# Performance work log

Hardware: AMD Instinct MI355X
Metric: run time of the kernel (lower is better)

The kernel has to match this reference:

```python
import jax, jax.numpy as jnp
import numpy as np

B_SZ, L, D, N = 2, 2048, 1024, 16


def setup_inputs() -> dict:
    key = jax.random.key(0)
    ks = jax.random.split(key, 6)
    x = jax.random.normal(ks[0], (B_SZ, L, D), dtype=jnp.float32)
    W_b = jax.random.normal(ks[1], (N, D), dtype=jnp.float32) * (1.0 / np.sqrt(D))
    W_c = jax.random.normal(ks[2], (N, D), dtype=jnp.float32) * (1.0 / np.sqrt(D))
    # scaled so softplus(s_delta) stays in a sane range (avoids exp overflow)
    W_delta = jax.random.normal(ks[3], (1, D), dtype=jnp.float32) * 0.02
    # negative A (standard for stable SSMs) keeps exp(Delta*A) bounded
    A = -jnp.abs(jax.random.normal(ks[4], (D, N), dtype=jnp.float32))
    delta_param = jax.random.normal(ks[5], (D,), dtype=jnp.float32) * 0.1
    return {"x": x, "W_b": W_b, "W_c": W_c, "W_delta": W_delta, "A": A, "delta_param": delta_param}


def reference(x, W_b, W_c, W_delta, A, delta_param):
    # Input-dependent projections (torch Linear: x @ W.T)
    B = jnp.einsum("bld,nd->bln", x, W_b)                      # [b,l,n]
    C = jnp.einsum("bld,nd->bln", x, W_c)                      # [b,l,n]
    s_delta = jnp.einsum("bld,od->blo", x, W_delta)            # [b,l,1]
    # repeat_interleave(d) of a length-1 axis == broadcast over d
    Delta = jax.nn.softplus(s_delta + delta_param)             # [b,l,d]
    # ZOH discretization
    dA = Delta[..., None] * A                                  # [b,l,d,n]
    A_bar = jnp.exp(dA)                                        # [b,l,d,n]
    B_bar = (A_bar - 1.0) / dA * (Delta[..., None] * B[:, :, None, :])  # [b,l,d,n]
    deltaB_x = B_bar * x[..., None]                            # [b,l,d,n]
    # pack all computed quantities into one array: [b,l,2d+1,n]
    return jnp.concatenate([A_bar, deltaB_x, C[:, :, None, :]], axis=2)
```

## Files before the change

### kernel.cpp

```cpp
#include <hip/hip_runtime.h>
#include <cmath>

#define D_DIM 1024
#define N_DIM 16
#define KTOT  2049
#define WS_STRIDE 36

typedef float v4f __attribute__((ext_vector_type(4)));

__global__ __launch_bounds__(256) void proj_kernel(
    const float* __restrict__ x, const float* __restrict__ W_b,
    const float* __restrict__ W_c, const float* __restrict__ W_delta,
    float* __restrict__ ws, float* __restrict__ out)
{
    const int bl   = blockIdx.x;
    const int tid  = threadIdx.x;
    const int wave = tid >> 6;
    const int lane = tid & 63;

    const float* xrow  = x + (size_t)bl * D_DIM;
    const float* Wbase = (wave < 2) ? W_b : W_c;
    const int rowbase  = (wave & 1) * 8;

    float acc[8] = {0.f,0.f,0.f,0.f,0.f,0.f,0.f,0.f};
    float sd = 0.f;

    for (int i = 0; i < D_DIM / 64; ++i) {
        const int d = lane + (i << 6);
        const float xv = xrow[d];
        #pragma unroll
        for (int r = 0; r < 8; ++r)
            acc[r] = fmaf(xv, Wbase[(rowbase + r) * D_DIM + d], acc[r]);
        if (wave == 0) sd = fmaf(xv, W_delta[d], sd);
    }

    #pragma unroll
    for (int r = 0; r < 8; ++r) {
        #pragma unroll
        for (int m = 32; m >= 1; m >>= 1)
            acc[r] += __shfl_xor(acc[r], m, 64);
    }
    if (wave == 0) {
        #pragma unroll
        for (int m = 32; m >= 1; m >>= 1)
            sd += __shfl_xor(sd, m, 64);
    }

    if (lane == 0) {
        if (wave < 2) {
            float* dst = ws + (size_t)bl * WS_STRIDE + rowbase;
            #pragma unroll
            for (int r = 0; r < 8; ++r) dst[r] = acc[r];
            if (wave == 0) ws[(size_t)bl * WS_STRIDE + 32] = sd;
        } else {
            float* dst = out + ((size_t)bl * KTOT + 2 * D_DIM) * N_DIM + rowbase;
            #pragma unroll
            for (int r = 0; r < 8; ++r) dst[r] = acc[r];
        }
    }
}

__global__ __launch_bounds__(256) void ssm_kernel(
    const float* __restrict__ x, const float* __restrict__ A,
    const float* __restrict__ delta_param, const float* __restrict__ ws,
    float* __restrict__ out)
{
    const int blk   = blockIdx.x;
    const int bl    = blk >> 4;
    const int chunk = blk & 15;
    const int tid   = threadIdx.x;
    const int n4    = tid & 3;
    const int dloc  = tid >> 2;
    const int d     = (chunk << 6) + dloc;

    const float sd = ws[bl * WS_STRIDE + 32];
    const v4f   Bv = *(const v4f*)(ws + bl * WS_STRIDE + (n4 << 2));
    const float dp = delta_param[d];
    const v4f   Av = *(const v4f*)(A + (size_t)d * N_DIM + (n4 << 2));
    const float xv = x[(size_t)bl * D_DIM + d];

    const float z     = sd + dp;
    const float Delta = fmaxf(z, 0.0f) + log1pf(expf(-fabsf(z)));
    const float dx    = Delta * xv;

    v4f Abar, dbx;
    #pragma unroll
    for (int i = 0; i < 4; ++i) {
        const float dA = Delta * Av[i];
        const float em = expm1f(dA);
        Abar[i] = em + 1.0f;
        const float ratio = (dA != 0.0f) ? (em / dA) : 1.0f;
        dbx[i] = ratio * Bv[i] * dx;
    }

    const size_t base = ((size_t)bl * KTOT + d) * N_DIM + (n4 << 2);
    __builtin_nontemporal_store(Abar, (v4f*)(out + base));
    __builtin_nontemporal_store(dbx,  (v4f*)(out + base + (size_t)D_DIM * N_DIM));
}

extern "C" void kernel_launch(void* const* d_in, const int* in_sizes, int n_in,
                              void* d_out, int out_size, void* d_ws, size_t ws_size,
                              hipStream_t stream)
{
    const float* x           = (const float*)d_in[0];
    const float* W_b         = (const float*)d_in[1];
    const float* W_c         = (const float*)d_in[2];
    const float* W_delta     = (const float*)d_in[3];
    const float* A           = (const float*)d_in[4];
    const float* delta_param = (const float*)d_in[5];
    float* out = (float*)d_out;
    float* ws  = (float*)d_ws;

    const int BL = in_sizes[0] / D_DIM;

    proj_kernel<<<BL, 256, 0, stream>>>(x, W_b, W_c, W_delta, ws, out);
    ssm_kernel<<<BL * 16, 256, 0, stream>>>(x, A, delta_param, ws, out);
}
```

Measured before the change: 578.7 us.

## Fuse projection and SSM discretization into one kernel per token

Merges the projection kernel and the elementwise SSM kernel into a single launch per token. B and s_delta are passed through shared memory rather than a global workspace, and each block loops over all 16 d-chunks. The projection loads are vectorized to float4, and the softplus/exp/expm1 math uses hardware exp2/log/rcp intrinsics with a Taylor fallback for small dA. This removes one launch and the workspace round-trip. In exchange the grid shrinks to 4096 blocks each doing more serial work, and the math becomes slightly less accurate.

```diff
diff --git a/kernel.cpp b/kernel.cpp
--- a/kernel.cpp
+++ b/kernel.cpp
@@ -4,34 +4,49 @@
 #define D_DIM 1024
 #define N_DIM 16
 #define KTOT  2049
-#define WS_STRIDE 36
 
 typedef float v4f __attribute__((ext_vector_type(4)));
 
-__global__ __launch_bounds__(256) void proj_kernel(
+__global__ __launch_bounds__(256, 4) void fused_ssm_kernel(
     const float* __restrict__ x, const float* __restrict__ W_b,
     const float* __restrict__ W_c, const float* __restrict__ W_delta,
-    float* __restrict__ ws, float* __restrict__ out)
+    const float* __restrict__ A, const float* __restrict__ delta_param,
+    float* __restrict__ out)
 {
     const int bl   = blockIdx.x;
     const int tid  = threadIdx.x;
     const int wave = tid >> 6;
     const int lane = tid & 63;
 
-    const float* xrow  = x + (size_t)bl * D_DIM;
+    __shared__ float sB[17];
+
+    const float* xrow = x + (size_t)bl * D_DIM;
+
     const float* Wbase = (wave < 2) ? W_b : W_c;
     const int rowbase  = (wave & 1) * 8;
 
     float acc[8] = {0.f,0.f,0.f,0.f,0.f,0.f,0.f,0.f};
     float sd = 0.f;
 
-    for (int i = 0; i < D_DIM / 64; ++i) {
-        const int d = lane + (i << 6);
-        const float xv = xrow[d];
+    #pragma unroll
+    for (int i = 0; i < 4; ++i) {
+        const int d = (i << 8) + (lane << 2);
+        const v4f xv = *(const v4f*)(xrow + d);
         #pragma unroll
-        for (int r = 0; r < 8; ++r)
-            acc[r] = fmaf(xv, Wbase[(rowbase + r) * D_DIM + d], acc[r]);
-        if (wave == 0) sd = fmaf(xv, W_delta[d], sd);
+        for (int r = 0; r < 8; ++r) {
+            const v4f wv = *(const v4f*)(Wbase + (size_t)(rowbase + r) * D_DIM + d);
+            acc[r] = fmaf(xv.x, wv.x, acc[r]);
+            acc[r] = fmaf(xv.y, wv.y, acc[r]);
+            acc[r] = fmaf(xv.z, wv.z, acc[r]);
+            acc[r] = fmaf(xv.w, wv.w, acc[r]);
+        }
+        if (wave == 0) {
+            const v4f wd = *(const v4f*)(W_delta + d);
+            sd = fmaf(xv.x, wd.x, sd);
+            sd = fmaf(xv.y, wd.y, sd);
+            sd = fmaf(xv.z, wd.z, sd);
+            sd = fmaf(xv.w, wd.w, sd);
+        }
     }
 
     #pragma unroll
@@ -47,55 +62,58 @@
     }
 
     if (lane == 0) {
-        if (wave < 2) {
-            float* dst = ws + (size_t)bl * WS_STRIDE + rowbase;
+        if (wave == 0) {
             #pragma unroll
-            for (int r = 0; r < 8; ++r) dst[r] = acc[r];
-            if (wave == 0) ws[(size_t)bl * WS_STRIDE + 32] = sd;
+            for (int r = 0; r < 8; ++r) sB[r] = acc[r];
+            sB[16] = sd;
+        } else if (wave == 1) {
+            #pragma unroll
+            for (int r = 0; r < 8; ++r) sB[8 + r] = acc[r];
         } else {
             float* dst = out + ((size_t)bl * KTOT + 2 * D_DIM) * N_DIM + rowbase;
             #pragma unroll
             for (int r = 0; r < 8; ++r) dst[r] = acc[r];
         }
     }
-}
+    __syncthreads();
 
-__global__ __launch_bounds__(256) void ssm_kernel(
-    const float* __restrict__ x, const float* __restrict__ A,
-    const float* __restrict__ delta_param, const float* __restrict__ ws,
-    float* __restrict__ out)
-{
-    const int blk   = blockIdx.x;
-    const int bl    = blk >> 4;
-    const int chunk = blk & 15;
-    const int tid   = threadIdx.x;
-    const int n4    = tid & 3;
-    const int dloc  = tid >> 2;
-    const int d     = (chunk << 6) + dloc;
+    const int n4   = tid & 3;
+    const int dloc = tid >> 2;
+    const v4f   Bv  = *(const v4f*)(sB + (n4 << 2));
+    const float sdv = sB[16];
+    const size_t tokbase = (size_t)bl * KTOT * N_DIM;
+    const float LOG2E = 1.44269504088896340736f;
 
-    const float sd = ws[bl * WS_STRIDE + 32];
-    const v4f   Bv = *(const v4f*)(ws + bl * WS_STRIDE + (n4 << 2));
-    const float dp = delta_param[d];
-    const v4f   Av = *(const v4f*)(A + (size_t)d * N_DIM + (n4 << 2));
-    const float xv = x[(size_t)bl * D_DIM + d];
+    #pragma unroll 4
+    for (int chunk = 0; chunk < 16; ++chunk) {
+        const int d = (chunk << 6) + dloc;
+        const float dp = delta_param[d];
+        const v4f   Av = *(const v4f*)(A + (size_t)d * N_DIM + (n4 << 2));
+        const float xv = xrow[d];
 
-    const float z     = sd + dp;
-    const float Delta = fmaxf(z, 0.0f) + log1pf(expf(-fabsf(z)));
-    const float dx    = Delta * xv;
+        const float z  = sdv + dp;
+        const float ez = __builtin_amdgcn_exp2f(-fabsf(z) * LOG2E);
+        const float Delta = fmaxf(z, 0.0f) +
+                            __builtin_amdgcn_logf(1.0f + ez) * 0.69314718055994530942f;
+        const float dx = Delta * xv;
 
-    v4f Abar, dbx;
-    #pragma unroll
-    for (int i = 0; i < 4; ++i) {
-        const float dA = Delta * Av[i];
-        const float em = expm1f(dA);
-        Abar[i] = em + 1.0f;
-        const float ratio = (dA != 0.0f) ? (em / dA) : 1.0f;
-        dbx[i] = ratio * Bv[i] * dx;
+        v4f Abar, dbx;
+        #pragma unroll
+        for (int i = 0; i < 4; ++i) {
+            const float dA = Delta * Av[i];
+            const float ex = __builtin_amdgcn_exp2f(dA * LOG2E);
+            const float em = ex - 1.0f;
+            const float r_big   = em * __builtin_amdgcn_rcpf(dA);
+            const float r_small = fmaf(dA, fmaf(dA, 0.16666667f, 0.5f), 1.0f);
+            const float ratio   = (fabsf(dA) < 0.03125f) ? r_small : r_big;
+            Abar[i] = ex;
+            dbx[i]  = ratio * Bv[i] * dx;
+        }
+
+        const size_t base = tokbase + (size_t)d * N_DIM + (n4 << 2);
+        __builtin_nontemporal_store(Abar, (v4f*)(out + base));
+        __builtin_nontemporal_store(dbx,  (v4f*)(out + base + (size_t)D_DIM * N_DIM));
     }
-
-    const size_t base = ((size_t)bl * KTOT + d) * N_DIM + (n4 << 2);
-    __builtin_nontemporal_store(Abar, (v4f*)(out + base));
-    __builtin_nontemporal_store(dbx,  (v4f*)(out + base + (size_t)D_DIM * N_DIM));
 }
 
 extern "C" void kernel_launch(void* const* d_in, const int* in_sizes, int n_in,
@@ -109,10 +127,8 @@
     const float* A           = (const float*)d_in[4];
     const float* delta_param = (const float*)d_in[5];
     float* out = (float*)d_out;
-    float* ws  = (float*)d_ws;
 
     const int BL = in_sizes[0] / D_DIM;
 
-    proj_kernel<<<BL, 256, 0, stream>>>(x, W_b, W_c, W_delta, ws, out);
-    ssm_kernel<<<BL * 16, 256, 0, stream>>>(x, A, delta_param, ws, out);
+    fused_ssm_kernel<<<BL, 256, 0, stream>>>(x, W_b, W_c, W_delta, A, delta_param, out);
 }
```

After: 600.2 us. 3.7% more time.
